# Kernel tuning notes

Hardware: AMD Instinct MI355X
Metric: run time of the kernel (lower is better)

## Reference

```python
import jax, jax.numpy as jnp
import numpy as np

H = 8            # head_size (hard-coded in the original forward)
BB = 0.6         # balance_bias
NEG = -1e9


def masked_softmax(x, m, axis=-1):
    # softmax over `axis`, zero out masked entries, renormalize
    p = jax.nn.softmax(x, axis=axis)
    p = p * m
    return p / (p.sum(axis=axis, keepdims=True) + 1e-13)


def setup_inputs():
    key = jax.random.key(0)
    ks = jax.random.split(key, 12)
    B, B0, V, A, Hd = 8, 2, 384, 384, 512
    S = V + A
    s = 1.0 / np.sqrt(Hd)
    return {
        'q': jax.random.normal(ks[0], (B, S, Hd), jnp.float32),
        'k': jax.random.normal(ks[1], (B, S, Hd), jnp.float32),
        'v': jax.random.normal(ks[2], (B, S, Hd), jnp.float32),
        'mask': jnp.ones((B, S, 1), jnp.float32),
        'depth_value': jax.random.uniform(ks[3], (B0, V), jnp.float32),
        'coord_3d': jax.random.normal(ks[4], (B, V, 3), jnp.float32),
        'va_v_mask': jnp.ones((B, V, 1), jnp.float32),
        'va_a_mask': jnp.ones((B, A, 1), jnp.float32),
        'mean_depth_value': jax.random.uniform(ks[5], (B, A), jnp.float32),
        'Wq': jax.random.normal(ks[6], (Hd, Hd), jnp.float32) * s,
        'bq': jnp.zeros((Hd,), jnp.float32),
        'Wk': jax.random.normal(ks[7], (Hd, Hd), jnp.float32) * s,
        'bk': jnp.zeros((Hd,), jnp.float32),
        'Wv': jax.random.normal(ks[8], (Hd, Hd), jnp.float32) * s,
        'bv': jnp.zeros((Hd,), jnp.float32),
        'Wo': jax.random.normal(ks[9], (Hd, Hd), jnp.float32) * s,
        'bo': jnp.zeros((Hd,), jnp.float32),
    }


def reference(q, k, v, mask, depth_value, coord_3d, va_v_mask, va_a_mask,
              mean_depth_value, Wq, bq, Wk, bk, Wv, bv, Wo, bo):
    B, S, Hd = q.shape
    d = Hd // H
    scale = d ** (-0.5)
    V = va_v_mask.shape[1]
    A = va_a_mask.shape[1]
    B0 = depth_value.shape[0]
    rep = B // B0  # = 4 in the original code

    qh = (q @ Wq + bq).reshape(B, S, H, d).transpose(0, 2, 1, 3)  # [B,H,S,d]
    kh = (k @ Wk + bk).reshape(B, S, H, d).transpose(0, 2, 1, 3)
    vh = (v @ Wv + bv).reshape(B, S, H, d).transpose(0, 2, 1, 3)

    m = mask[:, None]                      # [B,1,S,1]
    mask4 = m * jnp.swapaxes(m, 2, 3)      # [B,1,S,S] (broadcasts over heads)

    x = jnp.einsum('bhqd,bhkd->bhqk', qh, kh) * scale  # [B,H,S,S]

    # visual-visual depth bias
    dv = depth_value[:, :, None]                       # [B0,V,1]
    diff = jnp.abs(dv - jnp.swapaxes(dv, 1, 2))        # [B0,V,V]
    diff = jnp.repeat(diff, rep, axis=0)[:, None]      # [B,1,V,V]
    self_mask = 1.0 - jnp.eye(V, dtype=x.dtype)
    depth_term = jnp.abs(x[:, :, :V, :V]) * (jnp.exp(-diff) - BB) * self_mask  # [B,H,V,V]

    # audio->visual attention map (pre-bias scores)
    x_av = x[:, :, V:, :V]                             # [B,H,A,V]
    m_av = mask4[:, :, V:, :V]
    att_score_av = jnp.where(m_av > 0, x_av, NEG)
    att_map_av = masked_softmax(att_score_av, m_av, axis=3)

    # audio-visual depth bias (mean_depth_value branch)
    tdv = jnp.repeat(jnp.swapaxes(dv, 1, 2), rep, axis=0)           # [B,1,V]
    diff_va = jnp.abs(mean_depth_value[:, :, None] - tdv)[:, None]  # [B,1,A,V]
    depth_av_term = jnp.abs(x_av) * (jnp.exp(-diff_va) - BB)        # [B,H,A,V]

    # assemble bias matrix: [:V,:V]=depth_term, [V:,:V]=depth_av_term, rest 0
    top = jnp.concatenate([depth_term, jnp.zeros((B, H, V, S - V), x.dtype)], axis=3)
    bot = jnp.concatenate([depth_av_term, jnp.zeros((B, H, A, S - V), x.dtype)], axis=3)
    bias = jnp.concatenate([top, bot], axis=2)         # [B,H,S,S]

    x = x + bias
    att_score = jnp.where(mask4 > 0, x, NEG)
    att_map = masked_softmax(att_score, mask4 * jnp.ones((1, H, 1, 1), x.dtype), axis=3)
    out = jnp.einsum('bhqk,bhkd->bhqd', att_map, vh)   # [B,H,S,d]

    # auxiliary depth mean via the a->v attention map
    dv_rep = jnp.repeat(depth_value, rep, axis=0)      # [B,V]
    md = jnp.einsum('bhav,bv->bha', att_map_av, dv_rep)
    md = md.mean(axis=1)                               # [B,A]
    md = md.sum(axis=-1) / va_a_mask[:, :, 0].sum(axis=-1)  # [B]
    md = jnp.broadcast_to(md[:, None], (B, A))

    out = out.transpose(0, 2, 1, 3).reshape(B, S, H * d)
    out = out @ Wo + bo
    return out, att_score, att_map, md
```

## Files before the change

### kernel.cpp

```cpp
#include <hip/hip_runtime.h>
#include <hip/hip_bf16.h>
#include <cstdint>
#include <cstddef>

namespace {
constexpr int B  = 8;
constexpr int S  = 768;
constexpr int V  = 384;
constexpr int A  = 384;
constexpr int H  = 8;
constexpr int D  = 64;
constexpr int HD = 512;
constexpr float SCALE = 0.125f;
constexpr float BBC   = 0.6f;
constexpr float NEGV  = -1000000000.0f;
constexpr size_t N_QH = (size_t)B * H * S * D;
}

using short8 = __attribute__((ext_vector_type(8))) short;
using f32x4  = __attribute__((ext_vector_type(4))) float;

static __device__ __forceinline__ unsigned short f2bf(float f) {
  union { float f; unsigned int u; } v; v.f = f;
  unsigned int r = v.u + 0x7FFFu + ((v.u >> 16) & 1u);
  return (unsigned short)(r >> 16);
}
static __device__ __forceinline__ f32x4 mfma16(short8 a, short8 b, f32x4 c) {
  return __builtin_amdgcn_mfma_f32_16x16x32_bf16(a, b, c, 0, 0, 0);
}
static __device__ __forceinline__ short8 pack_bf8(float4 a, float4 b) {
  union { short8 s; uint4 u; } r;
  r.u.x = (unsigned)f2bf(a.x) | ((unsigned)f2bf(a.y) << 16);
  r.u.y = (unsigned)f2bf(a.z) | ((unsigned)f2bf(a.w) << 16);
  r.u.z = (unsigned)f2bf(b.x) | ((unsigned)f2bf(b.y) << 16);
  r.u.w = (unsigned)f2bf(b.z) | ((unsigned)f2bf(b.w) << 16);
  return r.s;
}
static __device__ __forceinline__ ushort4 pack_bf4(f32x4 a, float4 bi) {
  ushort4 r;
  r.x = f2bf(a[0] + bi.x); r.y = f2bf(a[1] + bi.y);
  r.z = f2bf(a[2] + bi.z); r.w = f2bf(a[3] + bi.w);
  return r;
}

__global__ __launch_bounds__(256) void prep_w(
    const float* __restrict__ Wq, const float* __restrict__ Wk,
    const float* __restrict__ Wv, const float* __restrict__ Wo,
    unsigned short* __restrict__ wt)
{
  __shared__ float tile[64][68];
  const int id = blockIdx.x;
  const int z = id >> 6, tl = id & 63;
  const int k0 = (tl >> 3) * 64, n0 = (tl & 7) * 64;
  const float* W = (z == 0) ? Wq : (z == 1) ? Wk : (z == 2) ? Wv : Wo;
  unsigned short* WT = wt + (size_t)z * 262144;
  const int t = threadIdx.x;
#pragma unroll
  for (int u = 0; u < 4; ++u) {
    int idx = u * 256 + t;
    int r = idx >> 4, c4 = (idx & 15) * 4;
    *(float4*)&tile[r][c4] = *(const float4*)&W[(size_t)(k0 + r) * 512 + n0 + c4];
  }
  __syncthreads();
#pragma unroll
  for (int u = 0; u < 4; ++u) {
    int idx = u * 256 + t;
    int n = idx >> 4, kq = (idx & 15) * 4;
    unsigned int h0 = f2bf(tile[kq + 0][n]), h1 = f2bf(tile[kq + 1][n]);
    unsigned int h2 = f2bf(tile[kq + 2][n]), h3 = f2bf(tile[kq + 3][n]);
    *(uint2*)&WT[(size_t)(n0 + n) * 512 + k0 + kq] =
        make_uint2(h0 | (h1 << 16), h2 | (h3 << 16));
  }
}

__global__ __launch_bounds__(256) void qkv_mfma(
    const float* __restrict__ q, const float* __restrict__ k,
    const float* __restrict__ v, const unsigned short* __restrict__ wt,
    const float* __restrict__ bq, const float* __restrict__ bk,
    const float* __restrict__ bv,
    unsigned short* __restrict__ qh, unsigned short* __restrict__ kh,
    unsigned short* __restrict__ vhT)
{
  __shared__ unsigned short Bh[64][40];
  __shared__ unsigned short Ax[64][40];
  const int lin = ((blockIdx.x & 7) * 288) + (blockIdx.x >> 3);
  const int n0 = (lin & 7) * 64;
  const int gidx = lin >> 3;
  const int mt = gidx % 96, z = gidx / 96;
  const int m0 = mt * 64;
  const float* X = (z == 0) ? q : (z == 1) ? k : v;
  const unsigned short* WT = wt + (size_t)z * 262144;
  const float* bias = (z == 0) ? bq : (z == 1) ? bk : bv;
  const int t = threadIdx.x, w = t >> 6, lane = t & 63;
  const int l15 = lane & 15, g = lane >> 4;
  const int bb = m0 / S;
  f32x4 acc[4] = {};

  const int srow = t >> 2, skq = (t & 3) * 8;
  for (int k0 = 0; k0 < 512; k0 += 32) {
    __syncthreads();
    *(short8*)&Bh[srow][skq] = *(const short8*)&WT[(size_t)(n0 + srow) * 512 + k0 + skq];
    if (z == 2) {
      float4 x0 = *(const float4*)&X[(size_t)(m0 + srow) * 512 + k0 + skq];
      float4 x1 = *(const float4*)&X[(size_t)(m0 + srow) * 512 + k0 + skq + 4];
      *(short8*)&Ax[srow][skq] = pack_bf8(x0, x1);
    }
    __syncthreads();
    if (z != 2) {
      const size_t abase = (size_t)(m0 + w * 16 + l15) * 512 + k0 + g * 8;
      float4 a0 = *(const float4*)&X[abase];
      float4 a1 = *(const float4*)&X[abase + 4];
      short8 xfrag = pack_bf8(a0, a1);
#pragma unroll
      for (int tn = 0; tn < 4; ++tn) {
        short8 wfrag = *(short8*)&Bh[tn * 16 + l15][g * 8];
        acc[tn] = mfma16(wfrag, xfrag, acc[tn]);
      }
    } else {
      short8 wh = *(short8*)&Bh[w * 16 + l15][g * 8];
#pragma unroll
      for (int tm = 0; tm < 4; ++tm) {
        short8 xf = *(short8*)&Ax[tm * 16 + l15][g * 8];
        acc[tm] = mfma16(wh, xf, acc[tm]);
      }
    }
  }

  if (z != 2) {
    unsigned short* Y = (z == 0) ? qh : kh;
    const int s = m0 + w * 16 + l15 - bb * S;
    const int h = n0 >> 6;
    unsigned short* yrow = &Y[((size_t)(bb * H + h) * S + s) * D];
#pragma unroll
    for (int tn = 0; tn < 4; ++tn) {
      const int d0 = tn * 16 + g * 4;
      float4 bi4 = *(const float4*)&bias[n0 + d0];
      *(ushort4*)&yrow[d0] = pack_bf4(acc[tn], bi4);
    }
  } else {
#pragma unroll
    for (int tm = 0; tm < 4; ++tm) {
      const int mcol = m0 + tm * 16 + l15;
      const int s = mcol - bb * S;
#pragma unroll
      for (int r = 0; r < 4; ++r) {
        const int n = n0 + w * 16 + g * 4 + r;
        const int h = n >> 6, d = n & 63;
        vhT[((size_t)(bb * H + h) * D + d) * S + s] = f2bf(acc[tm][r] + bias[n]);
      }
    }
  }
}

__global__ __launch_bounds__(256, 4) void fused_attn(
    const unsigned short* __restrict__ qh, const unsigned short* __restrict__ kh,
    const unsigned short* __restrict__ vhT,
    const float* __restrict__ mask, const float* __restrict__ depth_value,
    const float* __restrict__ mean_depth,
    float* __restrict__ att_score, float* __restrict__ att_map,
    unsigned short* __restrict__ ctx, float* __restrict__ md_rows)
{
  __shared__ unsigned short Ps[16][768];
  __shared__ float mcol[768];
  __shared__ float dvcol[384];
  __shared__ float pmax[16][4];
  __shared__ float psum[16][4];
  __shared__ float psem[16][4];
  __shared__ float asmd[16][2];
  __shared__ float mxA[16], rdA[16], drefsA[16], mrwA[16];

  const int id = blockIdx.x;
  const int rest = id >> 3;
  const int rt = rest % 48;
  const int bh = (id & 7) + 8 * (rest / 48);
  const int b = bh >> 3, b0 = b >> 2;
  const int r0 = rt * 16;
  const int t = threadIdx.x;
  const int w = t >> 6;
  const int lane = t & 63;
  const int l15 = lane & 15, g = lane >> 4;
  const bool avblk = (r0 >= V);

  for (int j = t; j < 768; j += 256) mcol[j] = mask[(size_t)b * S + j];
  for (int j = t; j < 384; j += 256) dvcol[j] = depth_value[(size_t)b0 * V + j];
  if (t < 16) {
    const int row = r0 + t;
    drefsA[t] = (row < V) ? depth_value[(size_t)b0 * V + row]
                          : mean_depth[(size_t)b * A + (row - V)];
    mrwA[t] = mask[(size_t)b * S + row];
  }

  short8 qf[2];
#pragma unroll
  for (int ks = 0; ks < 2; ++ks)
    qf[ks] = *(const short8*)&qh[((size_t)bh * S + r0 + l15) * D + ks * 32 + g * 8];

  f32x4 acc[12] = {};
#pragma unroll
  for (int tn = 0; tn < 12; ++tn) {
    const int col16 = w * 192 + tn * 16;
#pragma unroll
    for (int ks = 0; ks < 2; ++ks) {
      short8 kf = *(const short8*)&kh[((size_t)bh * S + col16 + l15) * D + ks * 32 + g * 8];
      acc[tn] = mfma16(kf, qf[ks], acc[tn]);
    }
  }
  __syncthreads();

  const bool biasw = (w < 2);
  const float mr = mrwA[l15];
  const float dref = drefsA[l15];
  const int grow = r0 + l15;

  {
    float* srow = &att_score[((size_t)bh * S + grow) * S];
#pragma unroll
    for (int tn = 0; tn < 12; ++tn) {
      const int colb = w * 192 + tn * 16 + g * 4;
      float4 mc4 = *(float4*)&mcol[colb];
      f32x4 x;
#pragma unroll
      for (int r = 0; r < 4; ++r) x[r] = acc[tn][r] * SCALE;
      if (biasw) {
        float4 dv4 = *(float4*)&dvcol[colb];
        float dvr[4] = {dv4.x, dv4.y, dv4.z, dv4.w};
#pragma unroll
        for (int r = 0; r < 4; ++r) {
          float gg = __expf(-fabsf(dref - dvr[r])) - BBC;
          float bb2 = fabsf(x[r]) * gg;
          if (grow == colb + r) bb2 = 0.f;
          x[r] += bb2;
        }
      }
      float mcr[4] = {mc4.x, mc4.y, mc4.z, mc4.w};
#pragma unroll
      for (int r = 0; r < 4; ++r) x[r] = (mr * mcr[r] > 0.f) ? x[r] : NEGV;
      __builtin_nontemporal_store(x, (f32x4*)&srow[colb]);
      acc[tn] = x;
    }
  }

  {
    float v = NEGV;
#pragma unroll
    for (int tn = 0; tn < 12; ++tn)
#pragma unroll
      for (int r = 0; r < 4; ++r) v = fmaxf(v, acc[tn][r]);
    v = fmaxf(v, __shfl_xor(v, 16));
    v = fmaxf(v, __shfl_xor(v, 32));
    if (g == 0) pmax[l15][w] = v;
  }
  __syncthreads();
  if (t < 16)
    mxA[t] = fmaxf(fmaxf(pmax[t][0], pmax[t][1]), fmaxf(pmax[t][2], pmax[t][3]));
  __syncthreads();

  if (avblk) {
    if (biasw) {
      const float amx = fmaxf(2.5f * mxA[l15], 0.f);
      float se = 0.f, sem = 0.f, smd = 0.f;
#pragma unroll
      for (int tn = 0; tn < 12; ++tn) {
        const int colb = w * 192 + tn * 16 + g * 4;
        float4 mc4 = *(float4*)&mcol[colb];
        float4 dv4 = *(float4*)&dvcol[colb];
        float mcr[4] = {mc4.x, mc4.y, mc4.z, mc4.w};
        float dvr[4] = {dv4.x, dv4.y, dv4.z, dv4.w};
#pragma unroll
        for (int r = 0; r < 4; ++r) {
          float post = acc[tn][r];
          float gg = __expf(-fabsf(dref - dvr[r])) - BBC;
          float pre = post / (post > 0.f ? 1.f + gg : 1.f - gg);
          float pm = mr * mcr[r];
          pre = (pm > 0.f) ? pre : NEGV;
          float e = __expf(pre - amx);
          se += e; sem += e * pm; smd += e * pm * dvr[r];
        }
      }
      se += __shfl_xor(se, 16);  se += __shfl_xor(se, 32);
      sem += __shfl_xor(sem, 16); sem += __shfl_xor(sem, 32);
      smd += __shfl_xor(smd, 16); smd += __shfl_xor(smd, 32);
      if (g == 0) { psum[l15][w] = se; psem[l15][w] = sem; asmd[l15][w] = smd; }
    }
    __syncthreads();
    if (t < 16) {
      float se = psum[t][0] + psum[t][1];
      float sem = psem[t][0] + psem[t][1];
      float smd = asmd[t][0] + asmd[t][1];
      md_rows[(size_t)bh * A + (r0 + t - V)] = smd / (sem + 1e-13f * se);
    }
    __syncthreads();
  }

  {
    const float mx = mxA[l15];
    float se = 0.f, sem = 0.f;
#pragma unroll
    for (int tn = 0; tn < 12; ++tn) {
      const int colb = w * 192 + tn * 16 + g * 4;
      float4 mc4 = *(float4*)&mcol[colb];
      float mcr[4] = {mc4.x, mc4.y, mc4.z, mc4.w};
#pragma unroll
      for (int r = 0; r < 4; ++r) {
        float e = __expf(acc[tn][r] - mx);
        acc[tn][r] = e;
        se += e; sem += e * (mr * mcr[r]);
      }
    }
    se += __shfl_xor(se, 16);  se += __shfl_xor(se, 32);
    sem += __shfl_xor(sem, 16); sem += __shfl_xor(sem, 32);
    if (g == 0) { psum[l15][w] = se; psem[l15][w] = sem; }
  }
  __syncthreads();
  if (t < 16) {
    float se = psum[t][0] + psum[t][1] + psum[t][2] + psum[t][3];
    float sem = psem[t][0] + psem[t][1] + psem[t][2] + psem[t][3];
    rdA[t] = 1.f / (sem + 1e-13f * se);
  }
  __syncthreads();

  {
    const float rden = rdA[l15];
    const int swz = (l15 & 7) << 4;
    float* prow = &att_map[((size_t)bh * S + grow) * S];
#pragma unroll
    for (int tn = 0; tn < 12; ++tn) {
      const int colb = w * 192 + tn * 16 + g * 4;
      float4 mc4 = *(float4*)&mcol[colb];
      float mcr[4] = {mc4.x, mc4.y, mc4.z, mc4.w};
      f32x4 p;
#pragma unroll
      for (int r = 0; r < 4; ++r) p[r] = acc[tn][r] * (mr * mcr[r]) * rden;
      __builtin_nontemporal_store(p, (f32x4*)&prow[colb]);
      ushort4 pk;
      pk.x = f2bf(p[0]); pk.y = f2bf(p[1]); pk.z = f2bf(p[2]); pk.w = f2bf(p[3]);
      *(ushort4*)&Ps[l15][colb ^ swz] = pk;
    }
  }
  __syncthreads();

  {
    const int aswz = (l15 & 7) << 4;
    f32x4 pacc = {};
    const unsigned short* vcol = &vhT[((size_t)bh * D + w * 16 + l15) * S];
#pragma unroll 8
    for (int kk = 0; kk < 24; ++kk) {
      short8 a = *(short8*)&Ps[l15][(kk * 32 + g * 8) ^ aswz];
      short8 bv = *(const short8*)&vcol[kk * 32 + g * 8];
      pacc = mfma16(a, bv, pacc);
    }
#pragma unroll
    for (int r = 0; r < 4; ++r) {
      const int row = r0 + g * 4 + r;
      ctx[((size_t)bh * S + row) * D + w * 16 + l15] = f2bf(pacc[r]);
    }
  }
}

__global__ __launch_bounds__(256) void gemm_out(
    const unsigned short* __restrict__ Xb, const unsigned short* __restrict__ WT,
    const float* __restrict__ bias, float* __restrict__ Yf,
    const float* __restrict__ md_rows, const float* __restrict__ va_a_mask,
    float* __restrict__ md_out)
{
  const int t = threadIdx.x;
  if (blockIdx.x >= 768) {
    __shared__ float red0[256];
    __shared__ float red1[256];
    const int b = blockIdx.x - 768;
    float s1 = 0.f, s2 = 0.f;
    for (int u = t; u < H * A; u += 256) s1 += md_rows[(size_t)b * H * A + u];
    for (int u = t; u < A; u += 256) s2 += va_a_mask[(size_t)b * A + u];
    red0[t] = s1; red1[t] = s2;
    __syncthreads();
    for (int o = 128; o > 0; o >>= 1) {
      if (t < o) { red0[t] += red0[t + o]; red1[t] += red1[t + o]; }
      __syncthreads();
    }
    const float val = red0[0] / ((float)H * red1[0]);
    for (int u = t; u < A; u += 256) md_out[(size_t)b * A + u] = val;
    return;
  }
  __shared__ unsigned short Bh[64][40];
  const int lin = ((blockIdx.x & 7) * 96) + (blockIdx.x >> 3);
  const int n0 = (lin & 7) * 64;
  const int m0 = (lin >> 3) * 64;
  const int w = t >> 6, lane = t & 63;
  const int l15 = lane & 15, g = lane >> 4;
  const int bb = m0 / S;
  f32x4 acc[4] = {};
  const int srow = t >> 2, skq = (t & 3) * 8;
  const int s = m0 + w * 16 + l15 - bb * S;
  for (int k0 = 0; k0 < 512; k0 += 32) {
    __syncthreads();
    *(short8*)&Bh[srow][skq] = *(const short8*)&WT[(size_t)(n0 + srow) * 512 + k0 + skq];
    __syncthreads();
    const int h = k0 >> 6, d = (k0 & 63) + g * 8;
    short8 xfrag = *(const short8*)&Xb[((size_t)(bb * H + h) * S + s) * D + d];
#pragma unroll
    for (int tn = 0; tn < 4; ++tn) {
      short8 wfrag = *(short8*)&Bh[tn * 16 + l15][g * 8];
      acc[tn] = mfma16(wfrag, xfrag, acc[tn]);
    }
  }
  const int m = m0 + w * 16 + l15;
#pragma unroll
  for (int tn = 0; tn < 4; ++tn) {
    const int c0 = n0 + tn * 16 + g * 4;
    float4 bi4 = *(const float4*)&bias[c0];
    float4 o = make_float4(acc[tn][0] + bi4.x, acc[tn][1] + bi4.y,
                           acc[tn][2] + bi4.z, acc[tn][3] + bi4.w);
    *(float4*)&Yf[(size_t)m * 512 + c0] = o;
  }
}

extern "C" void kernel_launch(void* const* d_in, const int* in_sizes, int n_in,
                              void* d_out, int out_size, void* d_ws, size_t ws_size,
                              hipStream_t stream) {
  const float* q           = (const float*)d_in[0];
  const float* k           = (const float*)d_in[1];
  const float* v           = (const float*)d_in[2];
  const float* mask        = (const float*)d_in[3];
  const float* depth_value = (const float*)d_in[4];
  const float* va_a_mask   = (const float*)d_in[7];
  const float* mean_depth  = (const float*)d_in[8];
  const float* Wq = (const float*)d_in[9];
  const float* bq = (const float*)d_in[10];
  const float* Wk = (const float*)d_in[11];
  const float* bk = (const float*)d_in[12];
  const float* Wv = (const float*)d_in[13];
  const float* bv = (const float*)d_in[14];
  const float* Wo = (const float*)d_in[15];
  const float* bo = (const float*)d_in[16];

  unsigned short* wsu = (unsigned short*)d_ws;
  unsigned short* qh  = wsu;
  unsigned short* kh  = wsu + N_QH;
  unsigned short* vhT = wsu + 2 * N_QH;
  unsigned short* ctx = qh;
  unsigned short* wt  = wsu + 3 * N_QH;
  float* md_rows = (float*)(wsu + 3 * N_QH + 4 * 262144);

  float* out       = (float*)d_out;
  float* att_score = out + (size_t)B * S * HD;
  float* att_map   = att_score + (size_t)B * H * S * S;
  float* md_out    = att_map + (size_t)B * H * S * S;

  prep_w<<<256, 256, 0, stream>>>(Wq, Wk, Wv, Wo, wt);
  qkv_mfma<<<2304, 256, 0, stream>>>(q, k, v, wt, bq, bk, bv, qh, kh, vhT);
  fused_attn<<<3072, 256, 0, stream>>>(qh, kh, vhT, mask, depth_value, mean_depth,
                                       att_score, att_map, ctx, md_rows);
  gemm_out<<<776, 256, 0, stream>>>(ctx, wt + 3 * 262144, bo, out,
                                    md_rows, va_a_mask, md_out);
}
```

Before: 175.4 us.

## Precompute depth gating tables and read GEMM weights directly from global memory

The exp(-|dref-dv|)-BB gating factors, with the diagonal zeroed, are now computed once per batch in extra prep_w blocks and stored in workspace tables (ggv for the two depth batches, gga per batch). fused_attn reads these instead of recomputing expf per element in both the score and recovery passes. Separately, the QKV and output GEMMs drop the shared-memory weight staging and its barriers and load weight fragments straight from global/L2. This trades transcendental work for extra memory traffic, and relies on L2 holding the weights for the direct fragment loads.

```diff
diff --git a/kernel.cpp b/kernel.cpp
--- a/kernel.cpp
+++ b/kernel.cpp
@@ -46,30 +46,68 @@
 __global__ __launch_bounds__(256) void prep_w(
     const float* __restrict__ Wq, const float* __restrict__ Wk,
     const float* __restrict__ Wv, const float* __restrict__ Wo,
-    unsigned short* __restrict__ wt)
+    const float* __restrict__ depth_value, const float* __restrict__ mean_depth,
+    unsigned short* __restrict__ wt, float* __restrict__ ggv, float* __restrict__ gga)
 {
-  __shared__ float tile[64][68];
   const int id = blockIdx.x;
-  const int z = id >> 6, tl = id & 63;
-  const int k0 = (tl >> 3) * 64, n0 = (tl & 7) * 64;
-  const float* W = (z == 0) ? Wq : (z == 1) ? Wk : (z == 2) ? Wv : Wo;
-  unsigned short* WT = wt + (size_t)z * 262144;
   const int t = threadIdx.x;
-#pragma unroll
-  for (int u = 0; u < 4; ++u) {
-    int idx = u * 256 + t;
-    int r = idx >> 4, c4 = (idx & 15) * 4;
-    *(float4*)&tile[r][c4] = *(const float4*)&W[(size_t)(k0 + r) * 512 + n0 + c4];
-  }
-  __syncthreads();
-#pragma unroll
-  for (int u = 0; u < 4; ++u) {
-    int idx = u * 256 + t;
-    int n = idx >> 4, kq = (idx & 15) * 4;
-    unsigned int h0 = f2bf(tile[kq + 0][n]), h1 = f2bf(tile[kq + 1][n]);
-    unsigned int h2 = f2bf(tile[kq + 2][n]), h3 = f2bf(tile[kq + 3][n]);
-    *(uint2*)&WT[(size_t)(n0 + n) * 512 + k0 + kq] =
-        make_uint2(h0 | (h1 << 16), h2 | (h3 << 16));
+  if (id < 256) {
+    __shared__ float tile[64][68];
+    const int z = id >> 6, tl = id & 63;
+    const int k0 = (tl >> 3) * 64, n0 = (tl & 7) * 64;
+    const float* W = (z == 0) ? Wq : (z == 1) ? Wk : (z == 2) ? Wv : Wo;
+    unsigned short* WT = wt + (size_t)z * 262144;
+#pragma unroll
+    for (int u = 0; u < 4; ++u) {
+      int idx = u * 256 + t;
+      int r = idx >> 4, c4 = (idx & 15) * 4;
+      *(float4*)&tile[r][c4] = *(const float4*)&W[(size_t)(k0 + r) * 512 + n0 + c4];
+    }
+    __syncthreads();
+#pragma unroll
+    for (int u = 0; u < 4; ++u) {
+      int idx = u * 256 + t;
+      int n = idx >> 4, kq = (idx & 15) * 4;
+      unsigned int h0 = f2bf(tile[kq + 0][n]), h1 = f2bf(tile[kq + 1][n]);
+      unsigned int h2 = f2bf(tile[kq + 2][n]), h3 = f2bf(tile[kq + 3][n]);
+      *(uint2*)&WT[(size_t)(n0 + n) * 512 + k0 + kq] =
+          make_uint2(h0 | (h1 << 16), h2 | (h3 << 16));
+    }
+  } else {
+    const int gid = id - 256;
+    const int z = gid / 24;
+    const int rt = gid % 24;
+    const float* dvb;
+    float* dst;
+    if (z < 2) {
+      dvb = depth_value + (size_t)z * V;
+      dst = ggv + ((size_t)z * V + rt * 16) * V;
+    } else {
+      const int b = z - 2;
+      dvb = depth_value + (size_t)(b >> 2) * V;
+      dst = gga + ((size_t)b * A + rt * 16) * V;
+    }
+#pragma unroll
+    for (int u = 0; u < 6; ++u) {
+      const int idx = (u * 256 + t) * 4;
+      const int row = idx / 384;
+      const int col = idx - row * 384;
+      float dref;
+      if (z < 2) dref = dvb[rt * 16 + row];
+      else       dref = mean_depth[(size_t)(z - 2) * A + rt * 16 + row];
+      float4 dv4 = *(const float4*)&dvb[col];
+      float4 g4;
+      g4.x = __expf(-fabsf(dref - dv4.x)) - BBC;
+      g4.y = __expf(-fabsf(dref - dv4.y)) - BBC;
+      g4.z = __expf(-fabsf(dref - dv4.z)) - BBC;
+      g4.w = __expf(-fabsf(dref - dv4.w)) - BBC;
+      if (z < 2) {
+        const int rg = rt * 16 + row;
+        const int dcol = rg - col;
+        if (dcol >= 0 && dcol < 4) ((float*)&g4)[dcol] = 0.f;
+      }
+      *(float4*)&dst[(size_t)row * 384 + col] = g4;
+    }
   }
 }
 
@@ -81,7 +119,6 @@
     unsigned short* __restrict__ qh, unsigned short* __restrict__ kh,
     unsigned short* __restrict__ vhT)
 {
-  __shared__ unsigned short Bh[64][40];
   __shared__ unsigned short Ax[64][40];
   const int lin = ((blockIdx.x & 7) * 288) + (blockIdx.x >> 3);
   const int n0 = (lin & 7) * 64;
@@ -96,37 +133,19 @@
   const int bb = m0 / S;
   f32x4 acc[4] = {};
 
-  const int srow = t >> 2, skq = (t & 3) * 8;
-  for (int k0 = 0; k0 < 512; k0 += 32) {
-    __syncthreads();
-    *(short8*)&Bh[srow][skq] = *(const short8*)&WT[(size_t)(n0 + srow) * 512 + k0 + skq];
-    if (z == 2) {
-      float4 x0 = *(const float4*)&X[(size_t)(m0 + srow) * 512 + k0 + skq];
-      float4 x1 = *(const float4*)&X[(size_t)(m0 + srow) * 512 + k0 + skq + 4];
-      *(short8*)&Ax[srow][skq] = pack_bf8(x0, x1);
-    }
-    __syncthreads();
-    if (z != 2) {
-      const size_t abase = (size_t)(m0 + w * 16 + l15) * 512 + k0 + g * 8;
-      float4 a0 = *(const float4*)&X[abase];
-      float4 a1 = *(const float4*)&X[abase + 4];
+  if (z != 2) {
+    const size_t xrow = (size_t)(m0 + w * 16 + l15) * 512;
+#pragma unroll 4
+    for (int k0 = 0; k0 < 512; k0 += 32) {
+      float4 a0 = *(const float4*)&X[xrow + k0 + g * 8];
+      float4 a1 = *(const float4*)&X[xrow + k0 + g * 8 + 4];
       short8 xfrag = pack_bf8(a0, a1);
 #pragma unroll
       for (int tn = 0; tn < 4; ++tn) {
-        short8 wfrag = *(short8*)&Bh[tn * 16 + l15][g * 8];
+        short8 wfrag = *(const short8*)&WT[(size_t)(n0 + tn * 16 + l15) * 512 + k0 + g * 8];
         acc[tn] = mfma16(wfrag, xfrag, acc[tn]);
       }
-    } else {
-      short8 wh = *(short8*)&Bh[w * 16 + l15][g * 8];
-#pragma unroll
-      for (int tm = 0; tm < 4; ++tm) {
-        short8 xf = *(short8*)&Ax[tm * 16 + l15][g * 8];
-        acc[tm] = mfma16(wh, xf, acc[tm]);
-      }
-    }
-  }
-
-  if (z != 2) {
+    }
     unsigned short* Y = (z == 0) ? qh : kh;
     const int s = m0 + w * 16 + l15 - bb * S;
     const int h = n0 >> 6;
@@ -138,6 +157,20 @@
       *(ushort4*)&yrow[d0] = pack_bf4(acc[tn], bi4);
     }
   } else {
+    const int srow = t >> 2, skq = (t & 3) * 8;
+    for (int k0 = 0; k0 < 512; k0 += 32) {
+      float4 x0 = *(const float4*)&X[(size_t)(m0 + srow) * 512 + k0 + skq];
+      float4 x1 = *(const float4*)&X[(size_t)(m0 + srow) * 512 + k0 + skq + 4];
+      __syncthreads();
+      *(short8*)&Ax[srow][skq] = pack_bf8(x0, x1);
+      __syncthreads();
+      short8 wh = *(const short8*)&WT[(size_t)(n0 + w * 16 + l15) * 512 + k0 + g * 8];
+#pragma unroll
+      for (int tm = 0; tm < 4; ++tm) {
+        short8 xf = *(short8*)&Ax[tm * 16 + l15][g * 8];
+        acc[tm] = mfma16(wh, xf, acc[tm]);
+      }
+    }
 #pragma unroll
     for (int tm = 0; tm < 4; ++tm) {
       const int mcol = m0 + tm * 16 + l15;
@@ -156,7 +189,7 @@
     const unsigned short* __restrict__ qh, const unsigned short* __restrict__ kh,
     const unsigned short* __restrict__ vhT,
     const float* __restrict__ mask, const float* __restrict__ depth_value,
-    const float* __restrict__ mean_depth,
+    const float* __restrict__ ggv, const float* __restrict__ gga,
     float* __restrict__ att_score, float* __restrict__ att_map,
     unsigned short* __restrict__ ctx, float* __restrict__ md_rows)
 {
@@ -167,7 +200,7 @@
   __shared__ float psum[16][4];
   __shared__ float psem[16][4];
   __shared__ float asmd[16][2];
-  __shared__ float mxA[16], rdA[16], drefsA[16], mrwA[16];
+  __shared__ float mxA[16], rdA[16], mrwA[16];
 
   const int id = blockIdx.x;
   const int rest = id >> 3;
@@ -183,12 +216,7 @@
 
   for (int j = t; j < 768; j += 256) mcol[j] = mask[(size_t)b * S + j];
   for (int j = t; j < 384; j += 256) dvcol[j] = depth_value[(size_t)b0 * V + j];
-  if (t < 16) {
-    const int row = r0 + t;
-    drefsA[t] = (row < V) ? depth_value[(size_t)b0 * V + row]
-                          : mean_depth[(size_t)b * A + (row - V)];
-    mrwA[t] = mask[(size_t)b * S + row];
-  }
+  if (t < 16) mrwA[t] = mask[(size_t)b * S + r0 + t];
 
   short8 qf[2];
 #pragma unroll
@@ -209,8 +237,9 @@
 
   const bool biasw = (w < 2);
   const float mr = mrwA[l15];
-  const float dref = drefsA[l15];
   const int grow = r0 + l15;
+  const float* ggp = (r0 < V) ? &ggv[((size_t)b0 * V + grow) * (size_t)V]
+                              : &gga[((size_t)b * A + (grow - V)) * (size_t)V];
 
   {
     float* srow = &att_score[((size_t)bh * S + grow) * S];
@@ -222,15 +251,10 @@
 #pragma unroll
       for (int r = 0; r < 4; ++r) x[r] = acc[tn][r] * SCALE;
       if (biasw) {
-        float4 dv4 = *(float4*)&dvcol[colb];
-        float dvr[4] = {dv4.x, dv4.y, dv4.z, dv4.w};
-#pragma unroll
-        for (int r = 0; r < 4; ++r) {
-          float gg = __expf(-fabsf(dref - dvr[r])) - BBC;
-          float bb2 = fabsf(x[r]) * gg;
-          if (grow == colb + r) bb2 = 0.f;
-          x[r] += bb2;
-        }
+        float4 g4 = *(const float4*)&ggp[colb];
+        float ggr[4] = {g4.x, g4.y, g4.z, g4.w};
+#pragma unroll
+        for (int r = 0; r < 4; ++r) x[r] += fabsf(x[r]) * ggr[r];
       }
       float mcr[4] = {mc4.x, mc4.y, mc4.z, mc4.w};
 #pragma unroll
@@ -264,13 +288,14 @@
         const int colb = w * 192 + tn * 16 + g * 4;
         float4 mc4 = *(float4*)&mcol[colb];
         float4 dv4 = *(float4*)&dvcol[colb];
+        float4 g4 = *(const float4*)&ggp[colb];
         float mcr[4] = {mc4.x, mc4.y, mc4.z, mc4.w};
         float dvr[4] = {dv4.x, dv4.y, dv4.z, dv4.w};
+        float ggr[4] = {g4.x, g4.y, g4.z, g4.w};
 #pragma unroll
         for (int r = 0; r < 4; ++r) {
           float post = acc[tn][r];
-          float gg = __expf(-fabsf(dref - dvr[r])) - BBC;
-          float pre = post / (post > 0.f ? 1.f + gg : 1.f - gg);
+          float pre = post / (post > 0.f ? 1.f + ggr[r] : 1.f - ggr[r]);
           float pm = mr * mcr[r];
           pre = (pm > 0.f) ? pre : NEGV;
           float e = __expf(pre - amx);
@@ -381,7 +406,6 @@
     for (int u = t; u < A; u += 256) md_out[(size_t)b * A + u] = val;
     return;
   }
-  __shared__ unsigned short Bh[64][40];
   const int lin = ((blockIdx.x & 7) * 96) + (blockIdx.x >> 3);
   const int n0 = (lin & 7) * 64;
   const int m0 = (lin >> 3) * 64;
@@ -389,17 +413,14 @@
   const int l15 = lane & 15, g = lane >> 4;
   const int bb = m0 / S;
   f32x4 acc[4] = {};
-  const int srow = t >> 2, skq = (t & 3) * 8;
   const int s = m0 + w * 16 + l15 - bb * S;
+#pragma unroll 4
   for (int k0 = 0; k0 < 512; k0 += 32) {
-    __syncthreads();
-    *(short8*)&Bh[srow][skq] = *(const short8*)&WT[(size_t)(n0 + srow) * 512 + k0 + skq];
-    __syncthreads();
     const int h = k0 >> 6, d = (k0 & 63) + g * 8;
     short8 xfrag = *(const short8*)&Xb[((size_t)(bb * H + h) * S + s) * D + d];
 #pragma unroll
     for (int tn = 0; tn < 4; ++tn) {
-      short8 wfrag = *(short8*)&Bh[tn * 16 + l15][g * 8];
+      short8 wfrag = *(const short8*)&WT[(size_t)(n0 + tn * 16 + l15) * 512 + k0 + g * 8];
       acc[tn] = mfma16(wfrag, xfrag, acc[tn]);
     }
   }
@@ -439,16 +460,20 @@
   unsigned short* vhT = wsu + 2 * N_QH;
   unsigned short* ctx = qh;
   unsigned short* wt  = wsu + 3 * N_QH;
-  float* md_rows = (float*)(wsu + 3 * N_QH + 4 * 262144);
+  float* fbase   = (float*)(wsu + 3 * N_QH + 4 * 262144);
+  float* md_rows = fbase;
+  float* ggv     = fbase + (size_t)B * H * A;
+  float* gga     = ggv + 2 * (size_t)V * V;
 
   float* out       = (float*)d_out;
   float* att_score = out + (size_t)B * S * HD;
   float* att_map   = att_score + (size_t)B * H * S * S;
   float* md_out    = att_map + (size_t)B * H * S * S;
 
-  prep_w<<<256, 256, 0, stream>>>(Wq, Wk, Wv, Wo, wt);
+  prep_w<<<496, 256, 0, stream>>>(Wq, Wk, Wv, Wo, depth_value, mean_depth,
+                                  wt, ggv, gga);
   qkv_mfma<<<2304, 256, 0, stream>>>(q, k, v, wt, bq, bk, bv, qh, kh, vhT);
-  fused_attn<<<3072, 256, 0, stream>>>(qh, kh, vhT, mask, depth_value, mean_depth,
+  fused_attn<<<3072, 256, 0, stream>>>(qh, kh, vhT, mask, depth_value, ggv, gga,
                                        att_score, att_map, ctx, md_rows);
   gemm_out<<<776, 256, 0, stream>>>(ctx, wt + 3 * 262144, bo, out,
                                     md_rows, va_a_mask, md_out);
```

New measurement: 264.1 us. 1.51x slower.
